# Performance work log

Measured on AMD Instinct MI355X. Metric: run time of the kernel, lower is better.

The kernel has to match this reference:

```python
import jax, jax.numpy as jnp
import numpy as np

B, C, H, W = 8, 1, 1536, 2048
NUM_GTS = 64
GAMMA = 2.0        # standard FocalLoss(gamma=2), softmax + NLL with (1-pt)^gamma weight, mean reduction
LOSS_WEIGHT = 1.0


def setup_inputs() -> dict:
    key = jax.random.key(0)
    k1, k2, k3, k4, k5 = jax.random.split(key, 5)
    depth = jax.random.uniform(k1, (B, C, H, W), dtype=jnp.float32)
    # valid boxes: 1 <= tl, tl < br <= image bounds
    tl_x = jax.random.randint(k2, (NUM_GTS,), 1, W - 320)
    tl_y = jax.random.randint(k3, (NUM_GTS,), 1, H - 320)
    bw = jax.random.randint(k4, (NUM_GTS,), 32, 320)
    bh = jax.random.randint(k5, (NUM_GTS,), 32, 320)
    bbox_list = jnp.stack([tl_x, tl_y, tl_x + bw, tl_y + bh], axis=1).astype(jnp.int32)
    return {"depth": depth, "bbox_list": bbox_list, "device": 0}


def _overlap_mask(bbox_list, b, c, h, w):
    # Vectorized replacement for the per-box slice-assignment loop.
    tl_x, tl_y, br_x, br_y = (bbox_list[:, 0], bbox_list[:, 1], bbox_list[:, 2], bbox_list[:, 3])
    rows = jnp.arange(h)[None, :]  # [1, H]
    cols = jnp.arange(w)[None, :]  # [1, W]
    # First assignment in the original uses max(br_y, image_size[1]=C) and max(br_x, image_size[0]=B)
    br_y1 = jnp.maximum(br_y, c)
    br_x1 = jnp.maximum(br_x, b)
    row1 = ((rows >= (tl_y - 1)[:, None]) & (rows < br_y1[:, None])).astype(jnp.float32)  # [J, H]
    col1 = ((cols >= (tl_x - 1)[:, None]) & (cols < br_x1[:, None])).astype(jnp.float32)  # [J, W]
    # Second assignment: plain [tl_y-1:br_y, tl_x-1:br_x]
    row2 = ((rows >= (tl_y - 1)[:, None]) & (rows < br_y[:, None])).astype(jnp.float32)
    col2 = ((cols >= (tl_x - 1)[:, None]) & (cols < br_x[:, None])).astype(jnp.float32)
    # union over all boxes and both assignments via rank-J outer-product counts
    counts = row1.T @ col1 + row2.T @ col2  # [H, W]
    return counts > 0


def reference(depth, bbox_list, device):
    b, c, h, w = depth.shape
    mask = _overlap_mask(bbox_list, b, c, h, w)  # [H, W] bool, same for every (b, c)
    target = jnp.broadcast_to(mask[None, None], depth.shape).reshape(-1).astype(jnp.int32)  # [M]
    p = depth.reshape(-1)                          # [M]
    logits = jnp.stack([p, 1.0 - p], axis=1)       # [M, 2] = cat([depth, 1-depth]).permute(1,0)
    logpt = jax.nn.log_softmax(logits, axis=1)     # stable softmax+log once
    logpt_t = jnp.take_along_axis(logpt, target[:, None], axis=1)[:, 0]
    pt = jnp.exp(logpt_t)
    loss = jnp.mean(-((1.0 - pt) ** GAMMA) * logpt_t)
    return loss * LOSS_WEIGHT
```

## Files before the change

kernel.cpp:

```cpp
#include <hip/hip_runtime.h>

constexpr int Bn = 8, Hn = 1536, Wn = 2048;
constexpr int NUM_GTS = 64;
constexpr int PLANE   = Hn * Wn;
constexpr int GROUPS  = PLANE / 4;
constexpr int BLOCKS  = 1024;
constexpr int GSTRIDE = BLOCKS * 256;
constexpr float INV_N = 1.0f / (float)((long long)Bn * PLANE);

typedef float v2f __attribute__((ext_vector_type(2)));

__device__ __forceinline__ v2f pk_fma(v2f a, v2f b, v2f c) {
    v2f d;
    asm("v_pk_fma_f32 %0, %1, %2, %3" : "=v"(d) : "v"(a), "v"(b), "v"(c));
    return d;
}
__device__ __forceinline__ v2f pk_add(v2f a, v2f b) {
    v2f d;
    asm("v_pk_add_f32 %0, %1, %2" : "=v"(d) : "v"(a), "v"(b));
    return d;
}

__device__ __forceinline__ v2f g_poly2(v2f x) {
    const float c0 = 0.173286795f, c1 = 0.298286795f, c2 = 0.199571699f,
                c3 = 0.048059430f, c4 = -0.011126533f, c5 = -0.007670527f,
                c6 = 0.000523747f, c7 = 0.001047450f, c8 = 0.000015192f;
    v2f t = (v2f){c8, c8};
    t = pk_fma(t, x, (v2f){c7, c7});
    t = pk_fma(t, x, (v2f){c6, c6});
    t = pk_fma(t, x, (v2f){c5, c5});
    t = pk_fma(t, x, (v2f){c4, c4});
    t = pk_fma(t, x, (v2f){c3, c3});
    t = pk_fma(t, x, (v2f){c2, c2});
    t = pk_fma(t, x, (v2f){c1, c1});
    t = pk_fma(t, x, (v2f){c0, c0});
    return t;
}

__device__ __forceinline__ unsigned group_tbits(int r, int c0, int tly, int bry,
                                                const int* s_tlx, const int* s_brx) {
    const bool rowhit = (r >= tly - 1) && (r < bry);
    unsigned long long rowm = __ballot(rowhit);
    unsigned tb = 0u;
    while (rowm) {
        const int i = __ffsll((unsigned long long)rowm) - 1;
        rowm &= rowm - 1;
        int lo = s_tlx[i] - 1 - c0;
        int hi = s_brx[i] - c0;
        lo = lo < 0 ? 0 : lo;
        hi = hi > 4 ? 4 : hi;
        if (lo < hi) tb |= ((1u << hi) - (1u << lo));
    }
    return tb;
}

__global__ __launch_bounds__(256) void depth_loss_kernel(
    const float* __restrict__ depth,
    const int*   __restrict__ bbox,
    float*       __restrict__ ws)
{
    __shared__ int s_tlx[NUM_GTS], s_brx[NUM_GTS];
    const int tid = threadIdx.x;
    if (tid < NUM_GTS) {
        s_tlx[tid] = bbox[tid * 4 + 0];
        s_brx[tid] = bbox[tid * 4 + 2];
    }
    __syncthreads();

    const int lane = tid & 63;
    const int tly  = bbox[lane * 4 + 1];
    const int bry  = bbox[lane * 4 + 3];

    const int g0 = blockIdx.x * 256 + tid;
    const int g1 = g0 + GSTRIDE;
    const int g2 = g1 + GSTRIDE;

    const float* p0 = depth + (g0 << 2);
    const float* p1 = depth + (g1 << 2);
    const float* p2 = depth + (g2 << 2);

    const unsigned tbs[3] = {
        group_tbits(g0 >> 9, (g0 & 511) << 2, tly, bry, s_tlx, s_brx),
        group_tbits(g1 >> 9, (g1 & 511) << 2, tly, bry, s_tlx, s_brx),
        group_tbits(g2 >> 9, (g2 & 511) << 2, tly, bry, s_tlx, s_brx)};
    v2f s01[3], s23[3], n01[3], n23[3];
#pragma unroll
    for (int j = 0; j < 3; ++j) {
        const float sg0 = (tbs[j] & 1u) ? -1.0f : 1.0f;
        const float sg1 = (tbs[j] & 2u) ? -1.0f : 1.0f;
        const float sg2 = (tbs[j] & 4u) ? -1.0f : 1.0f;
        const float sg3 = (tbs[j] & 8u) ? -1.0f : 1.0f;
        s01[j] = (v2f){sg0, sg1};
        s23[j] = (v2f){sg2, sg3};
        n01[j] = (v2f){-2.0f * sg0, -2.0f * sg1};
        n23[j] = (v2f){-2.0f * sg2, -2.0f * sg3};
    }

#define LOAD3(dst, b)                                                          \
    do {                                                                       \
        dst[0] = *reinterpret_cast<const float4*>(p0 + (b) * PLANE);           \
        dst[1] = *reinterpret_cast<const float4*>(p1 + (b) * PLANE);           \
        dst[2] = *reinterpret_cast<const float4*>(p2 + (b) * PLANE);           \
    } while (0)

    float4 cur[3], nxt[3];
    LOAD3(cur, 0);

    v2f acc2 = (v2f){0.0f, 0.0f};
#pragma unroll
    for (int b = 0; b < Bn; ++b) {
        if (b + 1 < Bn) LOAD3(nxt, b + 1);
#pragma unroll
        for (int j = 0; j < 3; ++j) {
            const v2f q01 = (v2f){cur[j].x, cur[j].y};
            const v2f q23 = (v2f){cur[j].z, cur[j].w};
            acc2 = pk_add(acc2, g_poly2(pk_fma(n01[j], q01, s01[j])));
            acc2 = pk_add(acc2, g_poly2(pk_fma(n23[j], q23, s23[j])));
        }
#pragma unroll
        for (int j = 0; j < 3; ++j) cur[j] = nxt[j];
    }
    float acc = acc2.x + acc2.y;

#pragma unroll
    for (int off = 32; off > 0; off >>= 1)
        acc += __shfl_down(acc, off, 64);

    __shared__ float s_part[4];
    if (lane == 0) s_part[tid >> 6] = acc;
    __syncthreads();
    if (tid == 0)
        ws[blockIdx.x] = s_part[0] + s_part[1] + s_part[2] + s_part[3];
}

__global__ __launch_bounds__(64) void reduce_kernel(
    const float* __restrict__ ws,
    float*       __restrict__ out)
{
    const int tid = threadIdx.x;
    float s = 0.0f;
#pragma unroll
    for (int i = 0; i < 16; ++i)
        s += ws[tid + i * 64];
#pragma unroll
    for (int off = 32; off > 0; off >>= 1)
        s += __shfl_down(s, off, 64);
    if (tid == 0)
        out[0] = s * INV_N;
}

extern "C" void kernel_launch(void* const* d_in, const int* in_sizes, int n_in,
                              void* d_out, int out_size, void* d_ws, size_t ws_size,
                              hipStream_t stream) {
    const float* depth = (const float*)d_in[0];
    const int*   bbox  = (const int*)d_in[1];
    float*       out   = (float*)d_out;
    float*       ws    = (float*)d_ws;

    depth_loss_kernel<<<BLOCKS, 256, 0, stream>>>(depth, bbox, ws);
    reduce_kernel<<<1, 64, 0, stream>>>(ws, out);
}
```

Before: 24.78 us.

## Fuse final reduction into main kernel via last-block atomic counter and DPP sums

Replaces the separate reduce kernel launch with a last-block-done pattern: each block writes its partial sum, bumps a global atomic counter, and the final block reduces all partials and writes the output. Wave reductions switch from shuffles to DPP row/broadcast adds that leave the total in lane 63. This removes one kernel launch and its inter-kernel gap but adds a memset launch and relies on relaxed atomics plus a waitcnt for ordering, which may be fragile for memory visibility.

```diff
diff --git a/kernel.cpp b/kernel.cpp
--- a/kernel.cpp
+++ b/kernel.cpp
@@ -3,7 +3,6 @@
 constexpr int Bn = 8, Hn = 1536, Wn = 2048;
 constexpr int NUM_GTS = 64;
 constexpr int PLANE   = Hn * Wn;
-constexpr int GROUPS  = PLANE / 4;
 constexpr int BLOCKS  = 1024;
 constexpr int GSTRIDE = BLOCKS * 256;
 constexpr float INV_N = 1.0f / (float)((long long)Bn * PLANE);
@@ -37,6 +36,22 @@
     return t;
 }
 
+template <int CTRL, int RM>
+__device__ __forceinline__ float dpp_add(float x) {
+    const int t = __builtin_amdgcn_update_dpp(0, __float_as_int(x),
+                                              CTRL, RM, 0xF, true);
+    return x + __int_as_float(t);
+}
+__device__ __forceinline__ float wave_sum63(float x) {
+    x = dpp_add<0x111, 0xF>(x);
+    x = dpp_add<0x112, 0xF>(x);
+    x = dpp_add<0x114, 0xF>(x);
+    x = dpp_add<0x118, 0xF>(x);
+    x = dpp_add<0x142, 0xA>(x);
+    x = dpp_add<0x143, 0xC>(x);
+    return x;
+}
+
 __device__ __forceinline__ unsigned group_tbits(int r, int c0, int tly, int bry,
                                                 const int* s_tlx, const int* s_brx) {
     const bool rowhit = (r >= tly - 1) && (r < bry);
@@ -57,7 +72,9 @@
 __global__ __launch_bounds__(256) void depth_loss_kernel(
     const float* __restrict__ depth,
     const int*   __restrict__ bbox,
-    float*       __restrict__ ws)
+    float*       __restrict__ ws,
+    unsigned*    __restrict__ cnt,
+    float*       __restrict__ out)
 {
     __shared__ int s_tlx[NUM_GTS], s_brx[NUM_GTS];
     const int tid = threadIdx.x;
@@ -120,33 +137,37 @@
 #pragma unroll
         for (int j = 0; j < 3; ++j) cur[j] = nxt[j];
     }
-    float acc = acc2.x + acc2.y;
 
-#pragma unroll
-    for (int off = 32; off > 0; off >>= 1)
-        acc += __shfl_down(acc, off, 64);
+    float acc = wave_sum63(acc2.x + acc2.y);
 
     __shared__ float s_part[4];
-    if (lane == 0) s_part[tid >> 6] = acc;
+    __shared__ int   s_last;
+    if (lane == 63) s_part[tid >> 6] = acc;
     __syncthreads();
-    if (tid == 0)
-        ws[blockIdx.x] = s_part[0] + s_part[1] + s_part[2] + s_part[3];
-}
 
-__global__ __launch_bounds__(64) void reduce_kernel(
-    const float* __restrict__ ws,
-    float*       __restrict__ out)
-{
-    const int tid = threadIdx.x;
-    float s = 0.0f;
+    if (tid == 0) {
+        const float part = s_part[0] + s_part[1] + s_part[2] + s_part[3];
+        __hip_atomic_store(&ws[blockIdx.x], part,
+                           __ATOMIC_RELAXED, __HIP_MEMORY_SCOPE_AGENT);
+        asm volatile("s_waitcnt vmcnt(0)" ::: "memory");
+        const unsigned old = __hip_atomic_fetch_add(cnt, 1u,
+                           __ATOMIC_RELAXED, __HIP_MEMORY_SCOPE_AGENT);
+        s_last = (old == (unsigned)(BLOCKS - 1));
+    }
+    __syncthreads();
+
+    if (s_last) {
+        float s = 0.0f;
 #pragma unroll
-    for (int i = 0; i < 16; ++i)
-        s += ws[tid + i * 64];
-#pragma unroll
-    for (int off = 32; off > 0; off >>= 1)
-        s += __shfl_down(s, off, 64);
-    if (tid == 0)
-        out[0] = s * INV_N;
+        for (int k = 0; k < 4; ++k)
+            s += __hip_atomic_load(&ws[tid + k * 256],
+                                   __ATOMIC_RELAXED, __HIP_MEMORY_SCOPE_AGENT);
+        s = wave_sum63(s);
+        if (lane == 63) s_part[tid >> 6] = s;
+        __syncthreads();
+        if (tid == 0)
+            out[0] = (s_part[0] + s_part[1] + s_part[2] + s_part[3]) * INV_N;
+    }
 }
 
 extern "C" void kernel_launch(void* const* d_in, const int* in_sizes, int n_in,
@@ -156,7 +177,8 @@
     const int*   bbox  = (const int*)d_in[1];
     float*       out   = (float*)d_out;
     float*       ws    = (float*)d_ws;
+    unsigned*    cnt   = (unsigned*)((char*)d_ws + BLOCKS * sizeof(float));
 
-    depth_loss_kernel<<<BLOCKS, 256, 0, stream>>>(depth, bbox, ws);
-    reduce_kernel<<<1, 64, 0, stream>>>(ws, out);
+    hipMemsetAsync(cnt, 0, sizeof(unsigned), stream);
+    depth_loss_kernel<<<BLOCKS, 256, 0, stream>>>(depth, bbox, ws, cnt, out);
 }
```

New measurement: 35.85 us. 1.45x slower.
